# Performance work log

Hardware: AMD Instinct MI355X
Metric: run time of the kernel (lower is better)

The kernel has to match this reference:

```python
import jax, jax.numpy as jnp
import numpy as np

NUM_USERS = 100000
NUM_ITEMS = 50000
N = NUM_USERS + NUM_ITEMS
D = 64
L = 3
E = 2400000


def setup_inputs() -> dict:
    key = jax.random.key(0)
    ks = jax.random.split(key, 5)
    edge_index = jax.random.randint(ks[0], (2, E), 0, N, dtype=jnp.int32)
    user_emb = jax.random.normal(ks[1], (NUM_USERS, D), dtype=jnp.float32) * 0.1
    item_emb = jax.random.normal(ks[2], (NUM_ITEMS, D), dtype=jnp.float32) * 0.1
    Ws = jax.random.normal(ks[3], (L, D, D), dtype=jnp.float32) * (1.0 / np.sqrt(D))
    bs = jax.random.normal(ks[4], (L, D), dtype=jnp.float32) * 0.01
    return {"edge_index": edge_index, "user_emb": user_emb, "item_emb": item_emb,
            "Ws": Ws, "bs": bs}


def _gcn_conv(x, W, b, src, dst):
    # PyG GCNConv: h = x @ W; add self-loops; sym-normalize; aggregate at dst; + bias
    h = x @ W                                      # [N, D]
    loop = jnp.arange(N, dtype=src.dtype)
    s = jnp.concatenate([src, loop])               # [E+N]
    d = jnp.concatenate([dst, loop])
    ones = jnp.ones(s.shape[0], dtype=x.dtype)
    deg = jax.ops.segment_sum(ones, d, num_segments=N)          # in-degree incl. self-loop
    dinv = jnp.where(deg > 0, jax.lax.rsqrt(deg), 0.0)
    norm = dinv[s] * dinv[d]                       # [E+N]
    msg = h[s] * norm[:, None]                     # gather + scale  [E+N, D]
    out = jax.ops.segment_sum(msg, d, num_segments=N)            # scatter-add at dst
    return out + b


def reference(edge_index, user_emb, item_emb, Ws, bs):
    src, dst = edge_index[0], edge_index[1]
    x = jnp.concatenate([user_emb, item_emb], axis=0)  # [N, D]
    acc = x
    for l in range(L):
        x = _gcn_conv(x, Ws[l], bs[l], src, dst)
        acc = acc + x
    emb = acc / (L + 1)                              # mean over layer outputs
    return emb[:NUM_USERS], emb[NUM_USERS:]
```

## Files before the change

kernel.cpp:

```cpp
#include <hip/hip_runtime.h>

constexpr int D = 64;
constexpr int BUK_SHIFT = 9;
constexpr int BUK_NODES = 1 << BUK_SHIFT;
constexpr int MAX_NBUK = 320;
constexpr int TILE_E = 4096;

typedef __attribute__((ext_vector_type(8))) short short8;
typedef __attribute__((ext_vector_type(4))) float f32x4;

__device__ inline unsigned short f2bf(float f) {
    unsigned int u = __float_as_uint(f);
    u += 0x7FFFu + ((u >> 16) & 1u);
    return (unsigned short)(u >> 16);
}
__device__ inline float bf2f(unsigned short s) {
    return __uint_as_float(((unsigned int)s) << 16);
}

__global__ __launch_bounds__(256) void k_bucket_hist(const int* __restrict__ ei,
                                                     int* __restrict__ bcount,
                                                     int E, int nbuk) {
    __shared__ int h[MAX_NBUK];
    for (int i = threadIdx.x; i < nbuk; i += blockDim.x) h[i] = 0;
    __syncthreads();
    int stride = gridDim.x * blockDim.x;
    for (int e = blockIdx.x * blockDim.x + threadIdx.x; e < E; e += stride)
        atomicAdd(&h[ei[E + e] >> BUK_SHIFT], 1);
    __syncthreads();
    for (int i = threadIdx.x; i < nbuk; i += blockDim.x)
        if (h[i]) atomicAdd(&bcount[i], h[i]);
}

__global__ __launch_bounds__(512) void k_scan_buckets(const int* __restrict__ bcount,
                                                      int* __restrict__ bbase,
                                                      int* __restrict__ gfill,
                                                      int* __restrict__ rowptr,
                                                      int nbuk, int N, int E) {
    __shared__ int sc[512];
    int tid = threadIdx.x;
    int v = (tid < nbuk) ? bcount[tid] : 0;
    sc[tid] = v;
    __syncthreads();
    for (int off = 1; off < 512; off <<= 1) {
        int t = (tid >= off) ? sc[tid - off] : 0;
        __syncthreads();
        sc[tid] += t;
        __syncthreads();
    }
    if (tid < nbuk) { bbase[tid] = sc[tid] - v; gfill[tid] = 0; }
    if (tid == 0) { bbase[nbuk] = E; rowptr[N] = E; }
}

__global__ __launch_bounds__(512) void k_bucket_scatter(const int* __restrict__ ei,
                                                        const int* __restrict__ bbase,
                                                        int* __restrict__ gfill,
                                                        unsigned int* __restrict__ packed,
                                                        int E, int nbuk) {
    __shared__ int hist[MAX_NBUK], base[MAX_NBUK], fil[MAX_NBUK];
    const int tid = threadIdx.x;
    for (int i = tid; i < nbuk; i += 512) hist[i] = 0;
    __syncthreads();

    const int t0 = blockIdx.x * TILE_E;
    int bk[8];
    unsigned int vv[8];
#pragma unroll
    for (int j = 0; j < 8; ++j) {
        int e = t0 + tid + j * 512;
        bk[j] = -1;
        if (e < E) {
            int src = ei[e];
            int dst = ei[E + e];
            bk[j] = dst >> BUK_SHIFT;
            vv[j] = ((unsigned int)(dst & (BUK_NODES - 1)) << 18) | (unsigned int)src;
            atomicAdd(&hist[bk[j]], 1);
        }
    }
    __syncthreads();
    for (int i = tid; i < nbuk; i += 512) {
        if (hist[i]) base[i] = atomicAdd(&gfill[i], hist[i]);
        fil[i] = 0;
    }
    __syncthreads();
#pragma unroll
    for (int j = 0; j < 8; ++j) {
        if (bk[j] >= 0) {
            int b = bk[j];
            int pos = bbase[b] + base[b] + atomicAdd(&fil[b], 1);
            packed[pos] = vv[j];
        }
    }
}

__global__ __launch_bounds__(256) void k_build_csr(const unsigned int* __restrict__ packed,
                                                   const int* __restrict__ bbase,
                                                   int* __restrict__ rowptr,
                                                   float* __restrict__ dinv,
                                                   int* __restrict__ csr_src,
                                                   int N) {
    __shared__ int hist[BUK_NODES], rp[BUK_NODES], fil[BUK_NODES];
    const int b = blockIdx.x;
    const int s = bbase[b], t = bbase[b + 1];
    const int tid = threadIdx.x;
    for (int i = tid; i < BUK_NODES; i += 256) hist[i] = 0;
    __syncthreads();
    for (int e = s + tid; e < t; e += 256)
        atomicAdd(&hist[packed[e] >> 18], 1);
    __syncthreads();
    if (tid == 0) {
        int run = 0;
        for (int i = 0; i < BUK_NODES; ++i) { rp[i] = run; run += hist[i]; }
    }
    __syncthreads();
    const int dbase = b << BUK_SHIFT;
    for (int ld = tid; ld < BUK_NODES; ld += 256) {
        int d = dbase + ld;
        if (d < N) {
            rowptr[d] = s + rp[ld];
            dinv[d] = rsqrtf((float)(hist[ld] + 1));
        }
        fil[ld] = 0;
    }
    __syncthreads();
    for (int e = s + tid; e < t; e += 256) {
        unsigned int v = packed[e];
        int ld = v >> 18;
        int pos = s + rp[ld] + atomicAdd(&fil[ld], 1);
        csr_src[pos] = (int)(v & 0x3FFFFu);
    }
}

template <bool F32IN>
__global__ __launch_bounds__(256) void k_gemm(const float* __restrict__ u,
                                              const float* __restrict__ it,
                                              int U,
                                              const unsigned short* __restrict__ xin16,
                                              const float* __restrict__ W,
                                              const float* __restrict__ dinv,
                                              unsigned short* __restrict__ hs_out,
                                              int N) {
    const int lane = threadIdx.x & 63;
    const int g = lane >> 4;
    const int lr = lane & 15;

    short8 bf[4][2];
#pragma unroll
    for (int ct = 0; ct < 4; ++ct)
#pragma unroll
        for (int kb = 0; kb < 2; ++kb) {
            short8 v;
            int c = ct * 16 + lr;
#pragma unroll
            for (int e = 0; e < 4; ++e) {
                int k0 = kb * 32 + g * 4 + e;
                v[e]     = (short)f2bf(W[k0 * D + c]);
                v[e + 4] = (short)f2bf(W[(k0 + 16) * D + c]);
            }
            bf[ct][kb] = v;
        }

    const int wid = blockIdx.x * (blockDim.x >> 6) + (threadIdx.x >> 6);
    const int nw = gridDim.x * (blockDim.x >> 6);

    for (int rb = wid * 16; rb < N; rb += nw * 16) {
        int row = rb + lr;
        bool ok = (row < N);
        short8 af[2];
        if (F32IN) {
            const float* xr = nullptr;
            if (ok) xr = (row < U) ? (u + (size_t)row * D)
                                   : (it + (size_t)(row - U) * D);
#pragma unroll
            for (int kb = 0; kb < 2; ++kb) {
                float4 q0 = ok ? *(const float4*)(xr + kb * 32 + g * 4)
                               : float4{0.f, 0.f, 0.f, 0.f};
                float4 q1 = ok ? *(const float4*)(xr + kb * 32 + 16 + g * 4)
                               : float4{0.f, 0.f, 0.f, 0.f};
                short8 v;
                v[0] = (short)f2bf(q0.x); v[1] = (short)f2bf(q0.y);
                v[2] = (short)f2bf(q0.z); v[3] = (short)f2bf(q0.w);
                v[4] = (short)f2bf(q1.x); v[5] = (short)f2bf(q1.y);
                v[6] = (short)f2bf(q1.z); v[7] = (short)f2bf(q1.w);
                af[kb] = v;
            }
        } else {
            const unsigned short* xr = xin16 + (size_t)row * D;
#pragma unroll
            for (int kb = 0; kb < 2; ++kb) {
                short4 q0 = ok ? *(const short4*)(xr + kb * 32 + g * 4)
                               : short4{0, 0, 0, 0};
                short4 q1 = ok ? *(const short4*)(xr + kb * 32 + 16 + g * 4)
                               : short4{0, 0, 0, 0};
                short8 v;
                v[0] = q0.x; v[1] = q0.y; v[2] = q0.z; v[3] = q0.w;
                v[4] = q1.x; v[5] = q1.y; v[6] = q1.z; v[7] = q1.w;
                af[kb] = v;
            }
        }

        float di[4];
#pragma unroll
        for (int r = 0; r < 4; ++r) {
            int ro = rb + g * 4 + r;
            di[r] = (ro < N) ? dinv[ro] : 0.f;
        }

#pragma unroll
        for (int ct = 0; ct < 4; ++ct) {
            f32x4 a = {0.f, 0.f, 0.f, 0.f};
            a = __builtin_amdgcn_mfma_f32_16x16x32_bf16(af[0], bf[ct][0], a, 0, 0, 0);
            a = __builtin_amdgcn_mfma_f32_16x16x32_bf16(af[1], bf[ct][1], a, 0, 0, 0);
#pragma unroll
            for (int r = 0; r < 4; ++r) {
                int ro = rb + g * 4 + r;
                if (ro < N)
                    hs_out[(size_t)ro * D + ct * 16 + lr] = f2bf(a[r] * di[r]);
            }
        }
    }
}

template <bool LAST>
__global__ __launch_bounds__(256) void k_aggregate(const int* __restrict__ rowptr,
                                                   const int* __restrict__ csr_src,
                                                   const unsigned short* __restrict__ hs16,
                                                   const float* __restrict__ dinv,
                                                   const float* __restrict__ b,
                                                   unsigned short* __restrict__ val16,
                                                   const float* __restrict__ u,
                                                   const float* __restrict__ it,
                                                   int U,
                                                   const unsigned short* __restrict__ V1,
                                                   const unsigned short* __restrict__ V2,
                                                   float* __restrict__ acc,
                                                   int N) {
    int w = (int)((blockIdx.x * (size_t)blockDim.x + threadIdx.x) >> 6);
    int lane = threadIdx.x & 63;
    if (w >= N) return;
    const int half = lane >> 5;
    const int li = lane & 31;
    const unsigned int* T = (const unsigned int*)hs16;
    int beg = rowptr[w], end = rowptr[w + 1];
    const float di = dinv[w];

    float aLo[4] = {0.f, 0.f, 0.f, 0.f};
    float aHi[4] = {0.f, 0.f, 0.f, 0.f};
    if (half == 0) {
        unsigned int v = T[(size_t)w * 32 + li];
        aLo[0] += __uint_as_float(v << 16);
        aHi[0] += __uint_as_float(v & 0xffff0000u);
    }

    int e = beg;
    for (; e + 16 <= end; e += 16) {
        int idx[8];
#pragma unroll
        for (int j = 0; j < 8; ++j) idx[j] = csr_src[e + 2 * j + half];
        unsigned int g[8];
#pragma unroll
        for (int j = 0; j < 8; ++j) g[j] = T[(size_t)idx[j] * 32 + li];
#pragma unroll
        for (int j = 0; j < 8; ++j) {
            aLo[j & 3] += __uint_as_float(g[j] << 16);
            aHi[j & 3] += __uint_as_float(g[j] & 0xffff0000u);
        }
    }
    if (e + 8 <= end) {
        int idx[4];
#pragma unroll
        for (int j = 0; j < 4; ++j) idx[j] = csr_src[e + 2 * j + half];
        unsigned int g[4];
#pragma unroll
        for (int j = 0; j < 4; ++j) g[j] = T[(size_t)idx[j] * 32 + li];
#pragma unroll
        for (int j = 0; j < 4; ++j) {
            aLo[j] += __uint_as_float(g[j] << 16);
            aHi[j] += __uint_as_float(g[j] & 0xffff0000u);
        }
        e += 8;
    }
    for (int t2 = e + half; t2 < end; t2 += 2) {
        unsigned int g = T[(size_t)csr_src[t2] * 32 + li];
        aLo[0] += __uint_as_float(g << 16);
        aHi[0] += __uint_as_float(g & 0xffff0000u);
    }

    float sLo = (aLo[0] + aLo[1]) + (aLo[2] + aLo[3]);
    float sHi = (aHi[0] + aHi[1]) + (aHi[2] + aHi[3]);
    sLo += __shfl_xor(sLo, 32);
    sHi += __shfl_xor(sHi, 32);

    if (half == 0) {
        float2 bb = *(const float2*)(b + 2 * li);
        float vLo = fmaf(sLo, di, bb.x);
        float vHi = fmaf(sHi, di, bb.y);
        if (LAST) {
            const float* x0 = (w < U) ? (u + (size_t)w * D)
                                      : (it + (size_t)(w - U) * D);
            float2 x = *(const float2*)(x0 + 2 * li);
            unsigned int p1 = ((const unsigned int*)V1)[(size_t)w * 32 + li];
            unsigned int p2 = ((const unsigned int*)V2)[(size_t)w * 32 + li];
            float o0 = (x.x + __uint_as_float(p1 << 16)
                            + __uint_as_float(p2 << 16) + vLo) * 0.25f;
            float o1 = (x.y + __uint_as_float(p1 & 0xffff0000u)
                            + __uint_as_float(p2 & 0xffff0000u) + vHi) * 0.25f;
            *(float2*)(acc + (size_t)w * D + 2 * li) = float2{o0, o1};
        } else {
            unsigned int pk = ((unsigned int)f2bf(vHi) << 16) | (unsigned int)f2bf(vLo);
            ((unsigned int*)val16)[(size_t)w * 32 + li] = pk;
        }
    }
}

extern "C" void kernel_launch(void* const* d_in, const int* in_sizes, int n_in,
                              void* d_out, int out_size, void* d_ws, size_t ws_size,
                              hipStream_t stream) {
    const int* ei      = (const int*)d_in[0];
    const float* uemb  = (const float*)d_in[1];
    const float* iemb  = (const float*)d_in[2];
    const float* Ws    = (const float*)d_in[3];
    const float* bs    = (const float*)d_in[4];

    const int E = in_sizes[0] / 2;
    const int U = in_sizes[1] / D;
    const int I = in_sizes[2] / D;
    const int N = U + I;
    const int ND = N * D;
    const int nbuk = (N + BUK_NODES - 1) >> BUK_SHIFT;

    unsigned short* X  = (unsigned short*)d_ws;
    unsigned short* V1 = X + ND;
    unsigned short* V2 = V1 + ND;
    float* dinv    = (float*)(V2 + ND);
    int*   csr_src = (int*)(dinv + N);
    unsigned int* packed = (unsigned int*)(csr_src + E);
    int*   rowptr  = (int*)(packed + E);
    int*   bcount  = rowptr + N + 1;
    int*   bbase   = bcount + MAX_NBUK;
    int*   gfill   = bbase + MAX_NBUK + 1;

    float* acc = (float*)d_out;

    hipMemsetAsync(bcount, 0, nbuk * sizeof(int), stream);
    k_bucket_hist<<<512, 256, 0, stream>>>(ei, bcount, E, nbuk);
    k_scan_buckets<<<1, 512, 0, stream>>>(bcount, bbase, gfill, rowptr, nbuk, N, E);
    k_bucket_scatter<<<(E + TILE_E - 1) / TILE_E, 512, 0, stream>>>(ei, bbase, gfill,
                                                                   packed, E, nbuk);
    k_build_csr<<<nbuk, 256, 0, stream>>>(packed, bbase, rowptr, dinv, csr_src, N);

    const int nagg = (N + 3) / 4;
    k_gemm<true><<<1024, 256, 0, stream>>>(uemb, iemb, U, nullptr, Ws, dinv, X, N);
    k_aggregate<false><<<nagg, 256, 0, stream>>>(rowptr, csr_src, X, dinv, bs, V1,
                                                 nullptr, nullptr, U, nullptr, nullptr,
                                                 nullptr, N);
    k_gemm<false><<<1024, 256, 0, stream>>>(nullptr, nullptr, U, V1,
                                            Ws + (size_t)1 * D * D, dinv, X, N);
    k_aggregate<false><<<nagg, 256, 0, stream>>>(rowptr, csr_src, X, dinv, bs + D, V2,
                                                 nullptr, nullptr, U, nullptr, nullptr,
                                                 nullptr, N);
    k_gemm<false><<<1024, 256, 0, stream>>>(nullptr, nullptr, U, V2,
                                            Ws + (size_t)2 * D * D, dinv, X, N);
    k_aggregate<true><<<nagg, 256, 0, stream>>>(rowptr, csr_src, X, dinv, bs + 2 * D,
                                                nullptr, uemb, iemb, U, V1, V2, acc, N);
}
```

Baseline: 365.6 us.

## Quantize gathered node features to int8 with per-16-row scales

The GEMM output that the aggregation gathers is stored as unsigned 8-bit values plus one float scale per 16-row tile, instead of bf16. The aggregation kernel is reworked so each lane reads 4 bytes covering 4 features and four edges are handled in parallel per wavefront, with the 128 offset removed afterwards. This halves the bytes of the random neighbour gathers, which dominate the aggregation. In exchange it adds dequantization arithmetic and a scale load per edge, and costs accuracy through coarse 8-bit quantization.

```diff
diff --git a/kernel.cpp b/kernel.cpp
--- a/kernel.cpp
+++ b/kernel.cpp
@@ -17,6 +17,10 @@
 __device__ inline float bf2f(unsigned short s) {
     return __uint_as_float(((unsigned int)s) << 16);
 }
+__device__ inline float ub0(unsigned int q) { return (float)(q & 0xffu); }
+__device__ inline float ub1(unsigned int q) { return (float)((q >> 8) & 0xffu); }
+__device__ inline float ub2(unsigned int q) { return (float)((q >> 16) & 0xffu); }
+__device__ inline float ub3(unsigned int q) { return (float)(q >> 24); }
 
 __global__ __launch_bounds__(256) void k_bucket_hist(const int* __restrict__ ei,
                                                      int* __restrict__ bcount,
@@ -138,7 +142,8 @@
                                               const unsigned short* __restrict__ xin16,
                                               const float* __restrict__ W,
                                               const float* __restrict__ dinv,
-                                              unsigned short* __restrict__ hs_out,
+                                              unsigned char* __restrict__ X8,
+                                              float* __restrict__ S,
                                               int N) {
     const int lane = threadIdx.x & 63;
     const int g = lane >> 4;
@@ -206,6 +211,8 @@
             di[r] = (ro < N) ? dinv[ro] : 0.f;
         }
 
+        float vals[4][4];
+        float mx = 0.f;
 #pragma unroll
         for (int ct = 0; ct < 4; ++ct) {
             f32x4 a = {0.f, 0.f, 0.f, 0.f};
@@ -213,18 +220,34 @@
             a = __builtin_amdgcn_mfma_f32_16x16x32_bf16(af[1], bf[ct][1], a, 0, 0, 0);
 #pragma unroll
             for (int r = 0; r < 4; ++r) {
+                float v = a[r] * di[r];
+                vals[ct][r] = v;
+                mx = fmaxf(mx, fabsf(v));
+            }
+        }
+#pragma unroll
+        for (int off = 32; off > 0; off >>= 1)
+            mx = fmaxf(mx, __shfl_xor(mx, off));
+        mx = fmaxf(mx, 1e-30f);
+        const float sinv = 127.0f / mx;
+        if (lane == 0) S[rb >> 4] = mx * (1.0f / 127.0f);
+#pragma unroll
+        for (int ct = 0; ct < 4; ++ct)
+#pragma unroll
+            for (int r = 0; r < 4; ++r) {
                 int ro = rb + g * 4 + r;
                 if (ro < N)
-                    hs_out[(size_t)ro * D + ct * 16 + lr] = f2bf(a[r] * di[r]);
+                    X8[(size_t)ro * D + ct * 16 + lr] =
+                        (unsigned char)(int)(rintf(vals[ct][r] * sinv) + 128.f);
             }
-        }
     }
 }
 
 template <bool LAST>
 __global__ __launch_bounds__(256) void k_aggregate(const int* __restrict__ rowptr,
                                                    const int* __restrict__ csr_src,
-                                                   const unsigned short* __restrict__ hs16,
+                                                   const unsigned char* __restrict__ X8,
+                                                   const float* __restrict__ S,
                                                    const float* __restrict__ dinv,
                                                    const float* __restrict__ b,
                                                    unsigned short* __restrict__ val16,
@@ -238,77 +261,91 @@
     int w = (int)((blockIdx.x * (size_t)blockDim.x + threadIdx.x) >> 6);
     int lane = threadIdx.x & 63;
     if (w >= N) return;
-    const int half = lane >> 5;
-    const int li = lane & 31;
-    const unsigned int* T = (const unsigned int*)hs16;
+    const int es = lane >> 4;
+    const int lc = lane & 15;
+    const unsigned int* Q = (const unsigned int*)X8;
     int beg = rowptr[w], end = rowptr[w + 1];
     const float di = dinv[w];
 
-    float aLo[4] = {0.f, 0.f, 0.f, 0.f};
-    float aHi[4] = {0.f, 0.f, 0.f, 0.f};
-    if (half == 0) {
-        unsigned int v = T[(size_t)w * 32 + li];
-        aLo[0] += __uint_as_float(v << 16);
-        aHi[0] += __uint_as_float(v & 0xffff0000u);
+    float a0 = 0.f, a1 = 0.f, a2 = 0.f, a3 = 0.f, as = 0.f;
+    if (es == 0) {
+        unsigned int q = Q[(size_t)w * 16 + lc];
+        float s = S[w >> 4];
+        a0 = fmaf(ub0(q), s, a0); a1 = fmaf(ub1(q), s, a1);
+        a2 = fmaf(ub2(q), s, a2); a3 = fmaf(ub3(q), s, a3);
+        as += s;
     }
 
     int e = beg;
     for (; e + 16 <= end; e += 16) {
-        int idx[8];
-#pragma unroll
-        for (int j = 0; j < 8; ++j) idx[j] = csr_src[e + 2 * j + half];
-        unsigned int g[8];
-#pragma unroll
-        for (int j = 0; j < 8; ++j) g[j] = T[(size_t)idx[j] * 32 + li];
-#pragma unroll
-        for (int j = 0; j < 8; ++j) {
-            aLo[j & 3] += __uint_as_float(g[j] << 16);
-            aHi[j & 3] += __uint_as_float(g[j] & 0xffff0000u);
-        }
-    }
-    if (e + 8 <= end) {
         int idx[4];
 #pragma unroll
-        for (int j = 0; j < 4; ++j) idx[j] = csr_src[e + 2 * j + half];
-        unsigned int g[4];
-#pragma unroll
-        for (int j = 0; j < 4; ++j) g[j] = T[(size_t)idx[j] * 32 + li];
+        for (int j = 0; j < 4; ++j) idx[j] = csr_src[e + 4 * j + es];
+        unsigned int q[4];
+#pragma unroll
+        for (int j = 0; j < 4; ++j) q[j] = Q[(size_t)idx[j] * 16 + lc];
+        float s[4];
+#pragma unroll
+        for (int j = 0; j < 4; ++j) s[j] = S[idx[j] >> 4];
 #pragma unroll
         for (int j = 0; j < 4; ++j) {
-            aLo[j] += __uint_as_float(g[j] << 16);
-            aHi[j] += __uint_as_float(g[j] & 0xffff0000u);
-        }
-        e += 8;
-    }
-    for (int t2 = e + half; t2 < end; t2 += 2) {
-        unsigned int g = T[(size_t)csr_src[t2] * 32 + li];
-        aLo[0] += __uint_as_float(g << 16);
-        aHi[0] += __uint_as_float(g & 0xffff0000u);
-    }
-
-    float sLo = (aLo[0] + aLo[1]) + (aLo[2] + aLo[3]);
-    float sHi = (aHi[0] + aHi[1]) + (aHi[2] + aHi[3]);
-    sLo += __shfl_xor(sLo, 32);
-    sHi += __shfl_xor(sHi, 32);
-
-    if (half == 0) {
-        float2 bb = *(const float2*)(b + 2 * li);
-        float vLo = fmaf(sLo, di, bb.x);
-        float vHi = fmaf(sHi, di, bb.y);
+            a0 = fmaf(ub0(q[j]), s[j], a0);
+            a1 = fmaf(ub1(q[j]), s[j], a1);
+            a2 = fmaf(ub2(q[j]), s[j], a2);
+            a3 = fmaf(ub3(q[j]), s[j], a3);
+            as += s[j];
+        }
+    }
+    for (; e + 4 <= end; e += 4) {
+        int idx = csr_src[e + es];
+        unsigned int q = Q[(size_t)idx * 16 + lc];
+        float s = S[idx >> 4];
+        a0 = fmaf(ub0(q), s, a0); a1 = fmaf(ub1(q), s, a1);
+        a2 = fmaf(ub2(q), s, a2); a3 = fmaf(ub3(q), s, a3);
+        as += s;
+    }
+    int rem = end - e;
+    if (es < rem) {
+        int idx = csr_src[e + es];
+        unsigned int q = Q[(size_t)idx * 16 + lc];
+        float s = S[idx >> 4];
+        a0 = fmaf(ub0(q), s, a0); a1 = fmaf(ub1(q), s, a1);
+        a2 = fmaf(ub2(q), s, a2); a3 = fmaf(ub3(q), s, a3);
+        as += s;
+    }
+
+    const float bias128 = 128.f * as;
+    a0 -= bias128; a1 -= bias128; a2 -= bias128; a3 -= bias128;
+#pragma unroll
+    for (int off = 16; off <= 32; off <<= 1) {
+        a0 += __shfl_xor(a0, off);
+        a1 += __shfl_xor(a1, off);
+        a2 += __shfl_xor(a2, off);
+        a3 += __shfl_xor(a3, off);
+    }
+
+    if (es == 0) {
+        float4 bb = *(const float4*)(b + 4 * lc);
+        float v0 = fmaf(a0, di, bb.x);
+        float v1 = fmaf(a1, di, bb.y);
+        float v2 = fmaf(a2, di, bb.z);
+        float v3 = fmaf(a3, di, bb.w);
         if (LAST) {
             const float* x0 = (w < U) ? (u + (size_t)w * D)
                                       : (it + (size_t)(w - U) * D);
-            float2 x = *(const float2*)(x0 + 2 * li);
-            unsigned int p1 = ((const unsigned int*)V1)[(size_t)w * 32 + li];
-            unsigned int p2 = ((const unsigned int*)V2)[(size_t)w * 32 + li];
-            float o0 = (x.x + __uint_as_float(p1 << 16)
-                            + __uint_as_float(p2 << 16) + vLo) * 0.25f;
-            float o1 = (x.y + __uint_as_float(p1 & 0xffff0000u)
-                            + __uint_as_float(p2 & 0xffff0000u) + vHi) * 0.25f;
-            *(float2*)(acc + (size_t)w * D + 2 * li) = float2{o0, o1};
+            float4 x = *(const float4*)(x0 + 4 * lc);
+            ushort4 p1 = *(const ushort4*)(V1 + (size_t)w * D + 4 * lc);
+            ushort4 p2 = *(const ushort4*)(V2 + (size_t)w * D + 4 * lc);
+            float4 o;
+            o.x = (x.x + bf2f(p1.x) + bf2f(p2.x) + v0) * 0.25f;
+            o.y = (x.y + bf2f(p1.y) + bf2f(p2.y) + v1) * 0.25f;
+            o.z = (x.z + bf2f(p1.z) + bf2f(p2.z) + v2) * 0.25f;
+            o.w = (x.w + bf2f(p1.w) + bf2f(p2.w) + v3) * 0.25f;
+            *(float4*)(acc + (size_t)w * D + 4 * lc) = o;
         } else {
-            unsigned int pk = ((unsigned int)f2bf(vHi) << 16) | (unsigned int)f2bf(vLo);
-            ((unsigned int*)val16)[(size_t)w * 32 + li] = pk;
+            ushort4 pk;
+            pk.x = f2bf(v0); pk.y = f2bf(v1); pk.z = f2bf(v2); pk.w = f2bf(v3);
+            *(ushort4*)(val16 + (size_t)w * D + 4 * lc) = pk;
         }
     }
 }
@@ -328,9 +365,11 @@
     const int N = U + I;
     const int ND = N * D;
     const int nbuk = (N + BUK_NODES - 1) >> BUK_SHIFT;
-
-    unsigned short* X  = (unsigned short*)d_ws;
-    unsigned short* V1 = X + ND;
+    const int NT = (N + 15) / 16;
+
+    unsigned char* X8 = (unsigned char*)d_ws;
+    float* S = (float*)(X8 + ND);
+    unsigned short* V1 = (unsigned short*)(S + ((NT + 1) & ~1));
     unsigned short* V2 = V1 + ND;
     float* dinv    = (float*)(V2 + ND);
     int*   csr_src = (int*)(dinv + N);
@@ -350,17 +389,17 @@
     k_build_csr<<<nbuk, 256, 0, stream>>>(packed, bbase, rowptr, dinv, csr_src, N);
 
     const int nagg = (N + 3) / 4;
-    k_gemm<true><<<1024, 256, 0, stream>>>(uemb, iemb, U, nullptr, Ws, dinv, X, N);
-    k_aggregate<false><<<nagg, 256, 0, stream>>>(rowptr, csr_src, X, dinv, bs, V1,
+    k_gemm<true><<<1024, 256, 0, stream>>>(uemb, iemb, U, nullptr, Ws, dinv, X8, S, N);
+    k_aggregate<false><<<nagg, 256, 0, stream>>>(rowptr, csr_src, X8, S, dinv, bs, V1,
                                                  nullptr, nullptr, U, nullptr, nullptr,
                                                  nullptr, N);
     k_gemm<false><<<1024, 256, 0, stream>>>(nullptr, nullptr, U, V1,
-                                            Ws + (size_t)1 * D * D, dinv, X, N);
-    k_aggregate<false><<<nagg, 256, 0, stream>>>(rowptr, csr_src, X, dinv, bs + D, V2,
+                                            Ws + (size_t)1 * D * D, dinv, X8, S, N);
+    k_aggregate<false><<<nagg, 256, 0, stream>>>(rowptr, csr_src, X8, S, dinv, bs + D, V2,
                                                  nullptr, nullptr, U, nullptr, nullptr,
                                                  nullptr, N);
     k_gemm<false><<<1024, 256, 0, stream>>>(nullptr, nullptr, U, V2,
-                                            Ws + (size_t)2 * D * D, dinv, X, N);
-    k_aggregate<true><<<nagg, 256, 0, stream>>>(rowptr, csr_src, X, dinv, bs + 2 * D,
+                                            Ws + (size_t)2 * D * D, dinv, X8, S, N);
+    k_aggregate<true><<<nagg, 256, 0, stream>>>(rowptr, csr_src, X8, S, dinv, bs + 2 * D,
                                                 nullptr, uemb, iemb, U, V1, V2, acc, N);
 }
```

Measured after the change: 347.6 us. 1.05x faster.
